# Performance work log

Measured on AMD Instinct MI355X. Metric: run time of the kernel, lower is better.

Reference implementation:

```python
import jax, jax.numpy as jnp
import numpy as np
from jax import lax

L, S, H, D_IN, D_OUT = 4, 64, 256, 768, 768
B, T = 8, 2048
EPS = 1e-5


def _xavier(key, shape):
    fan_out, fan_in = shape[-2], shape[-1]
    limit = (6.0 / (fan_in + fan_out)) ** 0.5
    return jax.random.uniform(key, shape, jnp.float32, -limit, limit)


def setup_inputs() -> dict:
    key = jax.random.key(0)
    ks = jax.random.split(key, 12)
    return {
        "x": jax.random.normal(ks[0], (B, T, D_IN), jnp.float32),
        "in_proj_w": _xavier(ks[1], (H, D_IN)),
        "in_proj_b": jnp.zeros((H,), jnp.float32),
        "ln_g": jnp.ones((L, H), jnp.float32),
        "ln_b": jnp.zeros((L, H), jnp.float32),
        "ip_w": _xavier(ks[2], (L, S, H)),
        "ip_b": jnp.zeros((L, S), jnp.float32),
        "A": jax.random.normal(ks[3], (L, S, S), jnp.float32) * 0.1,
        "Bv": jax.random.normal(ks[4], (L, S), jnp.float32) * 0.1,
        "Cm": jax.random.normal(ks[5], (L, H, S), jnp.float32) * 0.1,
        "bias_A": jnp.zeros((L, S), jnp.float32),
        "bias_C": jnp.zeros((L, H), jnp.float32),
        "gate_w": _xavier(ks[6], (L, H, H)),
        "gate_b": jnp.zeros((L, H), jnp.float32),
        "proj_w": _xavier(ks[7], (L, H, H)),
        "proj_b": jnp.zeros((L, H), jnp.float32),
        "out_proj_w": _xavier(ks[8], (D_OUT, H)),
        "out_proj_b": jnp.zeros((D_OUT,), jnp.float32),
    }


def _layer_norm(x, g, b):
    mu = jnp.mean(x, axis=-1, keepdims=True)
    var = jnp.mean(jnp.square(x - mu), axis=-1, keepdims=True)
    return (x - mu) * lax.rsqrt(var + EPS) * g + b


def _ssm_layer(xn, ip_w, ip_b, A, Bv, Cm, bias_A, bias_C, gate_w, gate_b, proj_w, proj_b):
    # xn: [B, T, H]
    x_state = jnp.einsum("bth,sh->bts", xn, ip_w) + ip_b          # [B,T,S]
    gate = jax.nn.sigmoid(jnp.einsum("bth,gh->btg", xn, gate_w) + gate_b)  # [B,T,H]

    def step(h, xs_t):
        # h: [B,S], xs_t: [B,S]
        h = jnp.clip(h @ A.T + Bv * xs_t + bias_A, -10.0, 10.0)
        y = h @ Cm.T + bias_C                                     # [B,H]
        return h, y

    h0 = jnp.zeros((xn.shape[0], A.shape[0]), xn.dtype)
    _, ys = lax.scan(step, h0, jnp.swapaxes(x_state, 0, 1))        # ys: [T,B,H]
    y = jnp.swapaxes(ys, 0, 1)                                     # [B,T,H]
    y = jnp.einsum("bth,oh->bto", y, proj_w) + proj_b
    return gate * y + (1.0 - gate) * xn


def reference(x, in_proj_w, in_proj_b, ln_g, ln_b, ip_w, ip_b, A, Bv, Cm,
              bias_A, bias_C, gate_w, gate_b, proj_w, proj_b, out_proj_w, out_proj_b):
    h = jnp.einsum("btd,hd->bth", x, in_proj_w) + in_proj_b
    for i in range(L):
        xn = _layer_norm(h, ln_g[i], ln_b[i])
        h = h + _ssm_layer(xn, ip_w[i], ip_b[i], A[i], Bv[i], Cm[i],
                           bias_A[i], bias_C[i], gate_w[i], gate_b[i],
                           proj_w[i], proj_b[i])
    return jnp.einsum("bth,oh->bto", h, out_proj_w) + out_proj_b
```

## Files before the change

### kernel.cpp

```cpp
#include <hip/hip_runtime.h>

typedef float f32x4 __attribute__((ext_vector_type(4)));
typedef short short8 __attribute__((ext_vector_type(8)));

#define T_LEN 2048
#define HD 256
#define SD 64
#define DIN 768
#define DOUT 768
#define NCHUNK 32
#define CLEN 64

#define SBAR() __builtin_amdgcn_sched_barrier(0)

__device__ __forceinline__ unsigned short f2bf(float f) {
    unsigned int u = __float_as_uint(f);
    unsigned int r = u + 0x7FFFu + ((u >> 16) & 1u);
    return (unsigned short)(r >> 16);
}
__device__ __forceinline__ float bf2f(unsigned short h) {
    return __uint_as_float(((unsigned int)h) << 16);
}
__device__ __forceinline__ int swz(int row, int col, int stride) {
    return row * stride + (col ^ ((row & 7) << 3));
}
#define GLL(gp, lp) __builtin_amdgcn_global_load_lds( \
    (const __attribute__((address_space(1))) void*)(gp), \
    (__attribute__((address_space(3))) void*)(lp), 16, 0, 0)

__global__ __launch_bounds__(256) void cvt_w_k(const float* __restrict__ s0, const float* __restrict__ s1,
                                               const float* __restrict__ s2, const float* __restrict__ s3,
                                               const float* __restrict__ s4, const float* __restrict__ s5,
                                               unsigned short* __restrict__ d) {
    int i = blockIdx.x * 256 + threadIdx.x;
    if (i >= 1048576) return;
    float v;
    if (i < 196608)      v = s0[i];
    else if (i < 262144) v = s1[i - 196608];
    else if (i < 524288) v = s2[i - 262144];
    else if (i < 786432) v = s3[i - 524288];
    else if (i < 851968) v = s4[i - 786432];
    else                 v = s5[i - 851968];
    d[i] = f2bf(v);
}

__global__ __launch_bounds__(256) void matpow_k(const float* __restrict__ A, float* __restrict__ Apow) {
    __shared__ unsigned short Mh[4096], Ml[4096], MhT[4096], MlT[4096];
    const int l = blockIdx.x, tid = threadIdx.x;
    const int w = tid >> 6, ln = tid & 63, ll = ln & 15, lh = ln >> 4;
    const float* src = A + l * 4096;
    for (int i = tid; i < 4096; i += 256) {
        float v = src[i];
        unsigned short hi = f2bf(v);
        unsigned short lo = f2bf(v - bf2f(hi));
        int r = i >> 6, c = i & 63;
        Mh[swz(r, c, 64)] = hi;  Ml[swz(r, c, 64)] = lo;
        MhT[swz(c, r, 64)] = hi; MlT[swz(c, r, 64)] = lo;
    }
    __syncthreads();
    for (int it = 0; it < 6; it++) {
        f32x4 acc[4] = {};
#pragma unroll
        for (int ks = 0; ks < 2; ks++) {
            int ar = w * 16 + ll, c0 = ks * 32 + lh * 8;
            short8 ah = *reinterpret_cast<const short8*>(&Mh[swz(ar, c0, 64)]);
            short8 al = *reinterpret_cast<const short8*>(&Ml[swz(ar, c0, 64)]);
#pragma unroll
            for (int nf = 0; nf < 4; nf++) {
                int br = nf * 16 + ll;
                short8 bh = *reinterpret_cast<const short8*>(&MhT[swz(br, c0, 64)]);
                short8 bl = *reinterpret_cast<const short8*>(&MlT[swz(br, c0, 64)]);
                acc[nf] = __builtin_amdgcn_mfma_f32_16x16x32_bf16(ah, bh, acc[nf], 0, 0, 0);
                acc[nf] = __builtin_amdgcn_mfma_f32_16x16x32_bf16(ah, bl, acc[nf], 0, 0, 0);
                acc[nf] = __builtin_amdgcn_mfma_f32_16x16x32_bf16(al, bh, acc[nf], 0, 0, 0);
            }
        }
        __syncthreads();
#pragma unroll
        for (int nf = 0; nf < 4; nf++)
#pragma unroll
            for (int r = 0; r < 4; r++) {
                float v = acc[nf][r];
                int row = w * 16 + lh * 4 + r, col = nf * 16 + ll;
                unsigned short hi = f2bf(v);
                unsigned short lo = f2bf(v - bf2f(hi));
                Mh[swz(row, col, 64)] = hi;  Ml[swz(row, col, 64)] = lo;
                MhT[swz(col, row, 64)] = hi; MlT[swz(col, row, 64)] = lo;
            }
        __syncthreads();
    }
    for (int i = tid; i < 4096; i += 256) {
        int r = i >> 6, c = i & 63;
        Apow[l * 4096 + i] = bf2f(Mh[swz(r, c, 64)]) + bf2f(Ml[swz(r, c, 64)]);
    }
}

__global__ __launch_bounds__(256) void in_ln_k(const float* __restrict__ x,
                                               const unsigned short* __restrict__ w_in,
                                               const float* __restrict__ inb,
                                               const float* __restrict__ lng, const float* __restrict__ lnb,
                                               unsigned short* __restrict__ hb, unsigned short* __restrict__ xnb) {
    __shared__ unsigned short hnb[32 * 264];
    const int tid = threadIdx.x, l = tid & 63, w = tid >> 6;
    const int ll = l & 15, lh = l >> 4;
    const int mf = w >> 1, nh = w & 1;
    const int m0 = blockIdx.x * 32;
    const float* Ap = x + (size_t)(m0 + mf * 16 + ll) * DIN + lh * 8;
    const unsigned short* Wp = w_in + (size_t)(nh * 128 + ll) * DIN + lh * 8;
    f32x4 acc[8] = {};
#pragma unroll
    for (int kb = 0; kb < DIN; kb += 128) {
        float4 a0[4], a1[4];
#pragma unroll
        for (int ks = 0; ks < 4; ks++) {
            a0[ks] = *reinterpret_cast<const float4*>(Ap + kb + ks * 32);
            a1[ks] = *reinterpret_cast<const float4*>(Ap + kb + ks * 32 + 4);
        }
        short8 af[4];
#pragma unroll
        for (int ks = 0; ks < 4; ks++) {
            short8 t;
            t[0] = (short)f2bf(a0[ks].x); t[1] = (short)f2bf(a0[ks].y);
            t[2] = (short)f2bf(a0[ks].z); t[3] = (short)f2bf(a0[ks].w);
            t[4] = (short)f2bf(a1[ks].x); t[5] = (short)f2bf(a1[ks].y);
            t[6] = (short)f2bf(a1[ks].z); t[7] = (short)f2bf(a1[ks].w);
            af[ks] = t;
        }
#pragma unroll
        for (int half = 0; half < 2; half++) {
            short8 bfx[8][2];
#pragma unroll
            for (int ks = 0; ks < 2; ks++)
#pragma unroll
                for (int j = 0; j < 8; j++)
                    bfx[j][ks] = *reinterpret_cast<const short8*>(Wp + (size_t)(j * 16) * DIN + kb + (half * 2 + ks) * 32);
            SBAR();
#pragma unroll
            for (int ks = 0; ks < 2; ks++)
#pragma unroll
                for (int j = 0; j < 8; j++)
                    acc[j] = __builtin_amdgcn_mfma_f32_16x16x32_bf16(af[half * 2 + ks], bfx[j][ks], acc[j], 0, 0, 0);
        }
    }
#pragma unroll
    for (int j = 0; j < 8; j++)
#pragma unroll
        for (int r = 0; r < 4; r++) {
            int rowl = mf * 16 + lh * 4 + r;
            int col = nh * 128 + j * 16 + ll;
            hnb[rowl * 264 + col] = f2bf(acc[j][r] + inb[col]);
        }
    __syncthreads();
#pragma unroll
    for (int q = 0; q < 8; q++) {
        int rowl = w * 8 + q;
        size_t gidx = (size_t)(m0 + rowl) * HD + l * 4;
        ushort4 hv = *reinterpret_cast<const ushort4*>(&hnb[rowl * 264 + l * 4]);
        float o0 = bf2f(hv.x), o1 = bf2f(hv.y), o2 = bf2f(hv.z), o3 = bf2f(hv.w);
        float s = o0 + o1 + o2 + o3;
        float s2 = o0 * o0 + o1 * o1 + o2 * o2 + o3 * o3;
#pragma unroll
        for (int mm = 1; mm < 64; mm <<= 1) { s += __shfl_xor(s, mm); s2 += __shfl_xor(s2, mm); }
        float mean = s * (1.f / 256.f);
        float var = s2 * (1.f / 256.f) - mean * mean;
        float rstd = rsqrtf(var + 1e-5f);
        int c = l * 4;
        *reinterpret_cast<ushort4*>(hb + gidx) = hv;
        ushort4 xo;
        xo.x = f2bf((o0 - mean) * rstd * lng[c + 0] + lnb[c + 0]);
        xo.y = f2bf((o1 - mean) * rstd * lng[c + 1] + lnb[c + 1]);
        xo.z = f2bf((o2 - mean) * rstd * lng[c + 2] + lnb[c + 2]);
        xo.w = f2bf((o3 - mean) * rstd * lng[c + 3] + lnb[c + 3]);
        *reinterpret_cast<ushort4*>(xnb + gidx) = xo;
    }
}

__device__ __forceinline__ void staged_core256(const unsigned short* __restrict__ A, int m0b,
                                               const unsigned short* __restrict__ W, int n0,
                                               unsigned short* As, unsigned short* Bs,
                                               int tid, f32x4 (*acc)[4]) {
    const int l = tid & 63, w = tid >> 6;
    const int ll = l & 15, lh = l >> 4;
    const int lr = l >> 2, lc = (l & 3) * 8;
    const unsigned short* ga1 = A + (size_t)(m0b + w * 32 + lr) * 256 + lc;
    const unsigned short* ga2 = ga1 + 16 * 256;
    const unsigned short* gb  = W + (size_t)(n0 + w * 16 + lr) * 256 + lc;
    unsigned short* la1 = As + w * 1024;
    unsigned short* la2 = As + w * 1024 + 512;
    unsigned short* lb  = Bs + w * 512;
#pragma unroll
    for (int k0 = 0; k0 < 256; k0 += 32) {
        GLL(ga1 + k0, la1);
        GLL(ga2 + k0, la2);
        GLL(gb + k0, lb);
        __syncthreads();
        short8 a0 = *reinterpret_cast<const short8*>(&As[(w * 32 + ll) * 32 + lh * 8]);
        short8 a1 = *reinterpret_cast<const short8*>(&As[(w * 32 + 16 + ll) * 32 + lh * 8]);
        short8 b0 = *reinterpret_cast<const short8*>(&Bs[(ll) * 32 + lh * 8]);
        short8 b1 = *reinterpret_cast<const short8*>(&Bs[(16 + ll) * 32 + lh * 8]);
        short8 b2 = *reinterpret_cast<const short8*>(&Bs[(32 + ll) * 32 + lh * 8]);
        short8 b3 = *reinterpret_cast<const short8*>(&Bs[(48 + ll) * 32 + lh * 8]);
        acc[0][0] = __builtin_amdgcn_mfma_f32_16x16x32_bf16(a0, b0, acc[0][0], 0, 0, 0);
        acc[0][1] = __builtin_amdgcn_mfma_f32_16x16x32_bf16(a0, b1, acc[0][1], 0, 0, 0);
        acc[0][2] = __builtin_amdgcn_mfma_f32_16x16x32_bf16(a0, b2, acc[0][2], 0, 0, 0);
        acc[0][3] = __builtin_amdgcn_mfma_f32_16x16x32_bf16(a0, b3, acc[0][3], 0, 0, 0);
        acc[1][0] = __builtin_amdgcn_mfma_f32_16x16x32_bf16(a1, b0, acc[1][0], 0, 0, 0);
        acc[1][1] = __builtin_amdgcn_mfma_f32_16x16x32_bf16(a1, b1, acc[1][1], 0, 0, 0);
        acc[1][2] = __builtin_amdgcn_mfma_f32_16x16x32_bf16(a1, b2, acc[1][2], 0, 0, 0);
        acc[1][3] = __builtin_amdgcn_mfma_f32_16x16x32_bf16(a1, b3, acc[1][3], 0, 0, 0);
        __syncthreads();
    }
}

template <int N>
__global__ __launch_bounds__(256) void gemm_k(const unsigned short* __restrict__ A,
                                              const unsigned short* __restrict__ W,
                                              const float* __restrict__ bias,
                                              float* __restrict__ outf) {
    __shared__ char smem[128 * 68 * 4];
    unsigned short* As = (unsigned short*)smem;
    unsigned short* Bs = As + 4096;
    float* sf = (float*)smem;
    const int tid = threadIdx.x, l = tid & 63, w = tid >> 6;
    const int ll = l & 15, lh = l >> 4;
    const int m0b = blockIdx.x * 128;
    const int n0 = blockIdx.y * 64;
    f32x4 acc[2][4] = {};
    staged_core256(A, m0b, W, n0, As, Bs, tid, acc);
#pragma unroll
    for (int mf = 0; mf < 2; mf++)
#pragma unroll
        for (int nf = 0; nf < 4; nf++)
#pragma unroll
            for (int r = 0; r < 4; r++) {
                int rowl = w * 32 + mf * 16 + lh * 4 + r;
                int col = nf * 16 + ll;
                sf[rowl * 68 + col] = acc[mf][nf][r] + bias[n0 + col];
            }
    __syncthreads();
#pragma unroll
    for (int p = 0; p < 8; p++) {
        int rowl = p * 16 + (tid >> 4);
        int col = (tid & 15) * 4;
        f32x4 v = *reinterpret_cast<const f32x4*>(&sf[rowl * 68 + col]);
        __builtin_nontemporal_store(v, reinterpret_cast<f32x4*>(outf + (size_t)(m0b + rowl) * N + n0 + col));
    }
}

__global__ __launch_bounds__(256) void gateip_k(const unsigned short* __restrict__ xnb,
                                                const unsigned short* __restrict__ wg,
                                                const unsigned short* __restrict__ wip,
                                                const float* __restrict__ gbias, const float* __restrict__ ipb,
                                                const float* __restrict__ Bv, const float* __restrict__ bA,
                                                unsigned short* __restrict__ gB, float* __restrict__ u) {
    __shared__ char smem[128 * 68 * 4];
    unsigned short* As = (unsigned short*)smem;
    unsigned short* Bs = As + 4096;
    float* sf = (float*)smem;
    unsigned short* su = (unsigned short*)smem;
    const int tid = threadIdx.x, l = tid & 63, w = tid >> 6;
    const int ll = l & 15, lh = l >> 4;
    const int m0b = blockIdx.x * 128;
    const int y = blockIdx.y;
    const bool gate = (y < 4);
    const int n0 = gate ? y * 64 : 0;
    f32x4 acc[2][4] = {};
    staged_core256(xnb, m0b, gate ? wg : wip, n0, As, Bs, tid, acc);
    if (gate) {
#pragma unroll
        for (int mf = 0; mf < 2; mf++)
#pragma unroll
            for (int nf = 0; nf < 4; nf++)
#pragma unroll
                for (int r = 0; r < 4; r++) {
                    int rowl = w * 32 + mf * 16 + lh * 4 + r;
                    int col = nf * 16 + ll;
                    float v = acc[mf][nf][r] + gbias[n0 + col];
                    su[rowl * 72 + col] = f2bf(1.f / (1.f + __expf(-v)));
                }
        __syncthreads();
#pragma unroll
        for (int p = 0; p < 8; p++) {
            int rowl = p * 16 + (tid >> 4);
            int col = (tid & 15) * 4;
            ushort4 v = *reinterpret_cast<const ushort4*>(&su[rowl * 72 + col]);
            *reinterpret_cast<ushort4*>(gB + (size_t)(m0b + rowl) * HD + n0 + col) = v;
        }
    } else {
#pragma unroll
        for (int mf = 0; mf < 2; mf++)
#pragma unroll
            for (int nf = 0; nf < 4; nf++)
#pragma unroll
                for (int r = 0; r < 4; r++) {
                    int rowl = w * 32 + mf * 16 + lh * 4 + r;
                    int col = nf * 16 + ll;
                    float v = acc[mf][nf][r] + ipb[col];
                    sf[rowl * 68 + col] = Bv[col] * v + bA[col];
                }
        __syncthreads();
#pragma unroll
        for (int p = 0; p < 8; p++) {
            int rowl = p * 16 + (tid >> 4);
            int col = (tid & 15) * 4;
            int m = m0b + rowl;
            int t = m & 2047, b2 = m >> 11;
            float4 v = *reinterpret_cast<const float4*>(&sf[rowl * 68 + col]);
            *reinterpret_cast<float4*>(u + ((size_t)((t << 3) + b2)) * 64 + col) = v;
        }
    }
}

template <bool LAST>
__global__ __launch_bounds__(256) void post3_k(const unsigned short* __restrict__ Hs,
                                               const unsigned short* __restrict__ wc,
                                               const float* __restrict__ bC,
                                               const unsigned short* __restrict__ wp,
                                               const float* __restrict__ pb,
                                               const unsigned short* __restrict__ gB,
                                               unsigned short* __restrict__ xnb,
                                               unsigned short* __restrict__ hb,
                                               const float* __restrict__ lng2, const float* __restrict__ lnb2) {
    __shared__ unsigned short ys[32 * 256];
    __shared__ unsigned short hnb[32 * 264];
    const int tid = threadIdx.x, l = tid & 63, w = tid >> 6;
    const int ll = l & 15, lh = l >> 4;
    const int mf = w >> 1, nh = w & 1;
    const int m0 = blockIdx.x * 32;
    {
        short8 ha[2], cb[8][2];
        const unsigned short* Ap = Hs + (size_t)(m0 + mf * 16 + ll) * SD + lh * 8;
#pragma unroll
        for (int ks = 0; ks < 2; ks++)
            ha[ks] = *reinterpret_cast<const short8*>(Ap + ks * 32);
#pragma unroll
        for (int ks = 0; ks < 2; ks++)
#pragma unroll
            for (int j = 0; j < 8; j++)
                cb[j][ks] = *reinterpret_cast<const short8*>(wc + (size_t)((nh * 8 + j) * 16 + ll) * SD + ks * 32 + lh * 8);
        SBAR();
        f32x4 acc[8] = {};
#pragma unroll
        for (int ks = 0; ks < 2; ks++)
#pragma unroll
            for (int j = 0; j < 8; j++)
                acc[j] = __builtin_amdgcn_mfma_f32_16x16x32_bf16(ha[ks], cb[j][ks], acc[j], 0, 0, 0);
#pragma unroll
        for (int j = 0; j < 8; j++)
#pragma unroll
            for (int r = 0; r < 4; r++) {
                int rowl = mf * 16 + lh * 4 + r;
                int col = (nh * 8 + j) * 16 + ll;
                ys[swz(rowl, col, 256)] = f2bf(acc[j][r] + bC[col]);
            }
    }
    __syncthreads();
    {
        f32x4 acc2[8] = {};
        const int arow = mf * 16 + ll;
#pragma unroll
        for (int kb = 0; kb < 4; kb++) {
            short8 pwf[8][2];
#pragma unroll
            for (int ks = 0; ks < 2; ks++)
#pragma unroll
                for (int j = 0; j < 8; j++)
                    pwf[j][ks] = *reinterpret_cast<const short8*>(wp + (size_t)((nh * 8 + j) * 16 + ll) * HD + kb * 64 + ks * 32 + lh * 8);
            SBAR();
#pragma unroll
            for (int ks = 0; ks < 2; ks++) {
                int c0 = kb * 64 + ks * 32 + lh * 8;
                short8 a = *reinterpret_cast<const short8*>(&ys[swz(arow, c0, 256)]);
#pragma unroll
                for (int j = 0; j < 8; j++)
                    acc2[j] = __builtin_amdgcn_mfma_f32_16x16x32_bf16(a, pwf[j][ks], acc2[j], 0, 0, 0);
            }
        }
#pragma unroll
        for (int j = 0; j < 8; j++)
#pragma unroll
            for (int r = 0; r < 4; r++) {
                int rowl = mf * 16 + lh * 4 + r;
                int col = (nh * 8 + j) * 16 + ll;
                hnb[rowl * 264 + col] = f2bf(acc2[j][r] + pb[col]);
            }
    }
    __syncthreads();
#pragma unroll
    for (int q = 0; q < 8; q++) {
        int rowl = w * 8 + q;
        int m = m0 + rowl;
        int t = m >> 3, b2 = m & 7;
        size_t gidx = ((size_t)((b2 << 11) + t)) * HD + l * 4;
        ushort4 hv = *reinterpret_cast<const ushort4*>(hb + gidx);
        ushort4 gv = *reinterpret_cast<const ushort4*>(gB + gidx);
        ushort4 xv = *reinterpret_cast<const ushort4*>(xnb + gidx);
        ushort4 yv = *reinterpret_cast<const ushort4*>(&hnb[rowl * 264 + l * 4]);
        float g0 = bf2f(gv.x), g1 = bf2f(gv.y), g2 = bf2f(gv.z), g3 = bf2f(gv.w);
        float o0 = bf2f(hv.x) + g0 * bf2f(yv.x) + (1.f - g0) * bf2f(xv.x);
        float o1 = bf2f(hv.y) + g1 * bf2f(yv.y) + (1.f - g1) * bf2f(xv.y);
        float o2 = bf2f(hv.z) + g2 * bf2f(yv.z) + (1.f - g2) * bf2f(xv.z);
        float o3 = bf2f(hv.w) + g3 * bf2f(yv.w) + (1.f - g3) * bf2f(xv.w);
        ushort4 hbv;
        hbv.x = f2bf(o0); hbv.y = f2bf(o1); hbv.z = f2bf(o2); hbv.w = f2bf(o3);
        *reinterpret_cast<ushort4*>(hb + gidx) = hbv;
        if constexpr (!LAST) {
            float s = o0 + o1 + o2 + o3;
            float s2 = o0 * o0 + o1 * o1 + o2 * o2 + o3 * o3;
#pragma unroll
            for (int mm = 1; mm < 64; mm <<= 1) { s += __shfl_xor(s, mm); s2 += __shfl_xor(s2, mm); }
            float mean = s * (1.f / 256.f);
            float var = s2 * (1.f / 256.f) - mean * mean;
            float rstd = rsqrtf(var + 1e-5f);
            int c = l * 4;
            ushort4 xo;
            xo.x = f2bf((o0 - mean) * rstd * lng2[c + 0] + lnb2[c + 0]);
            xo.y = f2bf((o1 - mean) * rstd * lng2[c + 1] + lnb2[c + 1]);
            xo.z = f2bf((o2 - mean) * rstd * lng2[c + 2] + lnb2[c + 2]);
            xo.w = f2bf((o3 - mean) * rstd * lng2[c + 3] + lnb2[c + 3]);
            *reinterpret_cast<ushort4*>(xnb + gidx) = xo;
        }
    }
}

__device__ __forceinline__ void loadA64(const float* __restrict__ Af, int s, float* a) {
#pragma unroll
    for (int q = 0; q < 16; q++) {
        float4 v = reinterpret_cast<const float4*>(Af + s * 64)[q];
        a[q * 4 + 0] = v.x; a[q * 4 + 1] = v.y; a[q * 4 + 2] = v.z; a[q * 4 + 3] = v.w;
    }
}

__device__ __forceinline__ float step64(const float* a, float h, float uu) {
    float ac0 = uu, ac1 = 0.f, ac2 = 0.f, ac3 = 0.f;
#pragma unroll
    for (int k = 0; k < 64; k += 4) {
        float b0 = __int_as_float(__builtin_amdgcn_readlane(__float_as_int(h), k + 0));
        float b1 = __int_as_float(__builtin_amdgcn_readlane(__float_as_int(h), k + 1));
        float b2 = __int_as_float(__builtin_amdgcn_readlane(__float_as_int(h), k + 2));
        float b3 = __int_as_float(__builtin_amdgcn_readlane(__float_as_int(h), k + 3));
        ac0 = fmaf(b0, a[k + 0], ac0);
        ac1 = fmaf(b1, a[k + 1], ac1);
        ac2 = fmaf(b2, a[k + 2], ac2);
        ac3 = fmaf(b3, a[k + 3], ac3);
    }
    return (ac0 + ac1) + (ac2 + ac3);
}

__global__ __launch_bounds__(64) void scan_chunk_k(const float* __restrict__ Af,
                                                   const float* __restrict__ u,
                                                   float* __restrict__ Slast) {
    const int c = blockIdx.x >> 3, b = blockIdx.x & 7;
    const int s = threadIdx.x;
    float a[64];
    loadA64(Af, s, a);
    const float* up = u + (c * CLEN) * 512 + b * 64 + s;
    float uv[CLEN];
#pragma unroll
    for (int i = 0; i < CLEN; i++) uv[i] = up[i * 512];
    float h = 0.f;
#pragma unroll
    for (int i = 0; i < CLEN; i++) h = step64(a, h, uv[i]);
    Slast[blockIdx.x * 64 + s] = h;
}

__global__ __launch_bounds__(64) void replay_k(const float* __restrict__ Af,
                                               const float* __restrict__ Apow,
                                               const float* __restrict__ u,
                                               const float* __restrict__ Slast,
                                               unsigned short* __restrict__ Hs,
                                               int* __restrict__ flag) {
    const int c = blockIdx.x >> 3, b = blockIdx.x & 7;
    const int s = threadIdx.x;
    float a[64];
    float carry = 0.f;
    if (c > 0) {
        loadA64(Apow, s, a);
        for (int j = 0; j < c; j++) {
            float sl = Slast[(j * 8 + b) * 64 + s];
            carry = step64(a, carry, sl);
        }
    }
    loadA64(Af, s, a);
    const float* up = u + (c * CLEN) * 512 + b * 64 + s;
    float uv[CLEN];
#pragma unroll
    for (int i = 0; i < CLEN; i++) uv[i] = up[i * 512];
    float h = carry;
    unsigned short* hp = Hs + (c * CLEN) * 512 + b * 64 + s;
    bool bad = false;
#pragma unroll
    for (int i = 0; i < CLEN; i++) {
        h = step64(a, h, uv[i]);
        bad |= (fabsf(h) > 10.f);
        hp[i * 512] = f2bf(h);
    }
    if (__any(bad ? 1 : 0)) {
        if (s == 0) atomicOr(flag, 1);
    }
}

__global__ __launch_bounds__(64) void scan_seq_k(const float* __restrict__ Af,
                                                 const float* __restrict__ u,
                                                 unsigned short* __restrict__ Hs,
                                                 const int* __restrict__ flag) {
    if (*flag == 0) return;
    const int b = blockIdx.x;
    const int s = threadIdx.x;
    float a[64];
    loadA64(Af, s, a);
    float h = 0.f;
    for (int t = 0; t < T_LEN; t++) {
        float uu = u[((t << 3) + b) * 64 + s];
        float hp = step64(a, h, uu);
        h = fminf(fmaxf(hp, -10.f), 10.f);
        Hs[((t << 3) + b) * 64 + s] = f2bf(h);
    }
}

extern "C" void kernel_launch(void* const* d_in, const int* in_sizes, int n_in,
                              void* d_out, int out_size, void* d_ws, size_t ws_size,
                              hipStream_t stream) {
    const float* x    = (const float*)d_in[0];
    const float* inw  = (const float*)d_in[1];
    const float* inb  = (const float*)d_in[2];
    const float* lng  = (const float*)d_in[3];
    const float* lnb  = (const float*)d_in[4];
    const float* ipw  = (const float*)d_in[5];
    const float* ipb  = (const float*)d_in[6];
    const float* Amat = (const float*)d_in[7];
    const float* Bv   = (const float*)d_in[8];
    const float* Cm   = (const float*)d_in[9];
    const float* bA   = (const float*)d_in[10];
    const float* bC   = (const float*)d_in[11];
    const float* gw   = (const float*)d_in[12];
    const float* gbia = (const float*)d_in[13];
    const float* pw   = (const float*)d_in[14];
    const float* pb   = (const float*)d_in[15];
    const float* ow   = (const float*)d_in[16];
    const float* ob   = (const float*)d_in[17];

    char* ws = (char*)d_ws;
    float*          u  = (float*)(ws + 0);
    unsigned short* Hs = (unsigned short*)(ws + 4194304);
    unsigned short* hb = (unsigned short*)(ws + 14680064);
    unsigned short* wb = (unsigned short*)(ws + 25165824);
    unsigned short* xnb = (unsigned short*)(ws + 44040192);
    unsigned short* gB  = (unsigned short*)(ws + 52428800);

    char* sc = (char*)d_out;
    float* Apow  = (float*)(sc + 0);
    float* Slast = (float*)(sc + 65536);
    int*   flag  = (int*)(sc + 196608);

    const unsigned short* w_in = wb + 0;
    const unsigned short* w_ip = wb + 196608;
    const unsigned short* w_g  = wb + 262144;
    const unsigned short* w_p  = wb + 524288;
    const unsigned short* w_c  = wb + 786432;
    const unsigned short* w_o  = wb + 851968;

    hipMemsetAsync(flag, 0, 16, stream);
    cvt_w_k<<<4096, 256, 0, stream>>>(inw, ipw, gw, pw, Cm, ow, wb);
    matpow_k<<<4, 256, 0, stream>>>(Amat, Apow);

    in_ln_k<<<512, 256, 0, stream>>>(x, w_in, inb, lng, lnb, hb, xnb);
    for (int i = 0; i < 4; i++) {
        gateip_k<<<dim3(128, 5), 256, 0, stream>>>(xnb, w_g + i * 65536, w_ip + i * 16384,
                                                   gbia + i * HD, ipb + i * SD,
                                                   Bv + i * SD, bA + i * SD, gB, u);
        scan_chunk_k<<<256, 64, 0, stream>>>(Amat + i * 4096, u, Slast);
        replay_k<<<256, 64, 0, stream>>>(Amat + i * 4096, Apow + i * 4096, u, Slast, Hs, flag + i);
        scan_seq_k<<<8, 64, 0, stream>>>(Amat + i * 4096, u, Hs, flag + i);
        if (i < 3)
            post3_k<false><<<512, 256, 0, stream>>>(Hs, w_c + i * 16384, bC + i * HD,
                                                    w_p + i * 65536, pb + i * HD, gB, xnb, hb,
                                                    lng + (i + 1) * HD, lnb + (i + 1) * HD);
        else
            post3_k<true><<<512, 256, 0, stream>>>(Hs, w_c + i * 16384, bC + i * HD,
                                                   w_p + i * 65536, pb + i * HD, gB, xnb, hb,
                                                   lng, lnb);
    }
    gemm_k<DOUT><<<dim3(128, 12), 256, 0, stream>>>(hb, w_o, ob, (float*)d_out);
}
```

Measured before the change: 435.2 us.

## Stage input-projection weights through LDS via direct global-to-LDS loads

The input projection kernel now loads a 256x32 bf16 weight slice per k-step into shared memory cooperatively, using GLL (global-to-LDS) loads, instead of each wave reading its own weight fragments from global memory. This drops the redundant weight reads made by the two waves that share the same column half. The cost is two barriers per 32-wide k step with no double buffering, so load latency is no longer hidden by the earlier register prefetch of 128-wide k blocks. The LDS tile is unswizzled, so fragment reads may hit bank conflicts.

```diff
diff --git a/kernel.cpp b/kernel.cpp
--- a/kernel.cpp
+++ b/kernel.cpp
@@ -100,47 +100,35 @@
                                                const float* __restrict__ inb,
                                                const float* __restrict__ lng, const float* __restrict__ lnb,
                                                unsigned short* __restrict__ hb, unsigned short* __restrict__ xnb) {
-    __shared__ unsigned short hnb[32 * 264];
+    __shared__ unsigned short smem[8192 + 32 * 264];
+    unsigned short* Ws = smem;
+    unsigned short* hnb = smem + 8192;
     const int tid = threadIdx.x, l = tid & 63, w = tid >> 6;
     const int ll = l & 15, lh = l >> 4;
     const int mf = w >> 1, nh = w & 1;
     const int m0 = blockIdx.x * 32;
-    const float* Ap = x + (size_t)(m0 + mf * 16 + ll) * DIN + lh * 8;
-    const unsigned short* Wp = w_in + (size_t)(nh * 128 + ll) * DIN + lh * 8;
+    const float* ap = x + (size_t)(m0 + mf * 16 + ll) * DIN + lh * 8;
+    const unsigned short* gwb = w_in + (size_t)(w * 64 + (l >> 2)) * DIN + (l & 3) * 8;
+    unsigned short* lwb = &Ws[(w * 64) * 32];
     f32x4 acc[8] = {};
-#pragma unroll
-    for (int kb = 0; kb < DIN; kb += 128) {
-        float4 a0[4], a1[4];
-#pragma unroll
-        for (int ks = 0; ks < 4; ks++) {
-            a0[ks] = *reinterpret_cast<const float4*>(Ap + kb + ks * 32);
-            a1[ks] = *reinterpret_cast<const float4*>(Ap + kb + ks * 32 + 4);
-        }
-        short8 af[4];
-#pragma unroll
-        for (int ks = 0; ks < 4; ks++) {
-            short8 t;
-            t[0] = (short)f2bf(a0[ks].x); t[1] = (short)f2bf(a0[ks].y);
-            t[2] = (short)f2bf(a0[ks].z); t[3] = (short)f2bf(a0[ks].w);
-            t[4] = (short)f2bf(a1[ks].x); t[5] = (short)f2bf(a1[ks].y);
-            t[6] = (short)f2bf(a1[ks].z); t[7] = (short)f2bf(a1[ks].w);
-            af[ks] = t;
-        }
-#pragma unroll
-        for (int half = 0; half < 2; half++) {
-            short8 bfx[8][2];
-#pragma unroll
-            for (int ks = 0; ks < 2; ks++)
-#pragma unroll
-                for (int j = 0; j < 8; j++)
-                    bfx[j][ks] = *reinterpret_cast<const short8*>(Wp + (size_t)(j * 16) * DIN + kb + (half * 2 + ks) * 32);
-            SBAR();
-#pragma unroll
-            for (int ks = 0; ks < 2; ks++)
-#pragma unroll
-                for (int j = 0; j < 8; j++)
-                    acc[j] = __builtin_amdgcn_mfma_f32_16x16x32_bf16(af[half * 2 + ks], bfx[j][ks], acc[j], 0, 0, 0);
-        }
+    for (int k0 = 0; k0 < DIN; k0 += 32) {
+#pragma unroll
+        for (int q = 0; q < 4; q++)
+            GLL(gwb + (size_t)(q * 16) * DIN + k0, lwb + q * 16 * 32);
+        float4 a0 = *reinterpret_cast<const float4*>(ap + k0);
+        float4 a1 = *reinterpret_cast<const float4*>(ap + k0 + 4);
+        short8 af;
+        af[0] = (short)f2bf(a0.x); af[1] = (short)f2bf(a0.y);
+        af[2] = (short)f2bf(a0.z); af[3] = (short)f2bf(a0.w);
+        af[4] = (short)f2bf(a1.x); af[5] = (short)f2bf(a1.y);
+        af[6] = (short)f2bf(a1.z); af[7] = (short)f2bf(a1.w);
+        __syncthreads();
+#pragma unroll
+        for (int j = 0; j < 8; j++) {
+            short8 b = *reinterpret_cast<const short8*>(&Ws[(size_t)(nh * 128 + j * 16 + ll) * 32 + lh * 8]);
+            acc[j] = __builtin_amdgcn_mfma_f32_16x16x32_bf16(af, b, acc[j], 0, 0, 0);
+        }
+        __syncthreads();
     }
 #pragma unroll
     for (int j = 0; j < 8; j++)
```

Measured after the change: 408.0 us. 6.2% less time.
